# Optimization experiments

Measured on AMD Instinct MI355X. Metric: run time of the kernel, lower is better.

Reference implementation:

```python
import jax, jax.numpy as jnp
import numpy as np
from math import sqrt

L, H, D, HD, F, V, P = 8, 16, 1024, 64, 4096, 32000, 2048
B, S = 2, 2048
EPS = 1e-5


def _ln(x, g, b):
    m = jnp.mean(x, axis=-1, keepdims=True)
    v = jnp.mean((x - m) ** 2, axis=-1, keepdims=True)
    return (x - m) * jax.lax.rsqrt(v + EPS) * g + b


def setup_inputs() -> dict:
    key = jax.random.key(0)
    ks = jax.random.split(key, 12)
    w = 0.02
    return {
        'input_ids': jax.random.randint(ks[0], (B, S), 0, V),
        'tok_emb': jax.random.normal(ks[1], (V, D), jnp.float32) * w,
        'pos_emb': jax.random.normal(ks[2], (P, D), jnp.float32) * w,
        'emb_g': jnp.ones((D,), jnp.float32),
        'emb_b': jnp.zeros((D,), jnp.float32),
        'ln1_g': jnp.ones((L, D), jnp.float32),
        'ln1_b': jnp.zeros((L, D), jnp.float32),
        'ln2_g': jnp.ones((L, D), jnp.float32),
        'ln2_b': jnp.zeros((L, D), jnp.float32),
        'Wq': jax.random.normal(ks[3], (L, H, D, HD), jnp.float32) * w,
        'bq': jnp.zeros((L, H, HD), jnp.float32),
        'Wk': jax.random.normal(ks[4], (L, H, D, HD), jnp.float32) * w,
        'bk': jnp.zeros((L, H, HD), jnp.float32),
        'Wv': jax.random.normal(ks[5], (L, H, D, HD), jnp.float32) * w,
        'bv': jnp.zeros((L, H, HD), jnp.float32),
        'Wo': jax.random.normal(ks[6], (L, D, D), jnp.float32) * w,
        'bo': jnp.zeros((L, D), jnp.float32),
        'W1': jax.random.normal(ks[7], (L, D, F), jnp.float32) * w,
        'b1': jnp.zeros((L, F), jnp.float32),
        'W2': jax.random.normal(ks[8], (L, F, D), jnp.float32) * w,
        'b2': jnp.zeros((L, D), jnp.float32),
    }


def _encoder(input_ids, tok_emb, pos_emb, emb_g, emb_b, ln1_g, ln1_b, ln2_g,
             ln2_b, Wq, bq, Wk, bk, Wv, bv, Wo, bo, W1, b1, W2, b2):
    seq = input_ids.shape[-1]
    x = tok_emb[input_ids] + pos_emb[:seq][None, :, :]  # [B,S,D]
    x = _ln(x, emb_g, emb_b)  # dropout = identity (eval)

    scale = 1.0 / sqrt(HD)

    def layer(x, p):
        (g1, b1_, g2, b2_, wq, bq_, wk, bk_, wv, bv_, wo, bo_, w1, bb1, w2, bb2) = p
        h = _ln(x, g1, b1_)
        q = jnp.einsum('bsd,hdk->bhsk', h, wq) + bq_[:, None, :]
        k = jnp.einsum('bsd,hdk->bhsk', h, wk) + bk_[:, None, :]
        v = jnp.einsum('bsd,hdk->bhsk', h, wv) + bv_[:, None, :]
        scores = jnp.einsum('bhsk,bhtk->bhst', q, k) * scale
        w = jax.nn.softmax(scores, axis=-1)
        av = jnp.einsum('bhst,bhtk->bhsk', w, v)  # [B,H,S,hd]
        av = jnp.transpose(av, (0, 2, 1, 3)).reshape(x.shape[0], x.shape[1], D)
        x = x + jnp.einsum('bsd,de->bse', av, wo) + bo_
        h2 = _ln(x, g2, b2_)
        f = jax.nn.gelu(jnp.einsum('bsd,df->bsf', h2, w1) + bb1, approximate=False)
        x = x + jnp.einsum('bsf,fd->bsd', f, w2) + bb2
        return x, None

    xs = (ln1_g, ln1_b, ln2_g, ln2_b, Wq, bq, Wk, bk, Wv, bv, Wo, bo, W1, b1, W2, b2)
    x, _ = jax.lax.scan(layer, x, xs)
    return x


def reference(input_ids, tok_emb, pos_emb, emb_g, emb_b, ln1_g, ln1_b, ln2_g,
              ln2_b, Wq, bq, Wk, bk, Wv, bv, Wo, bo, W1, b1, W2, b2):
    return _encoder(input_ids, tok_emb, pos_emb, emb_g, emb_b, ln1_g, ln1_b,
                    ln2_g, ln2_b, Wq, bq, Wk, bk, Wv, bv, Wo, bo, W1, b1, W2, b2)
```

## Files before the change

### kernel.cpp

```cpp
#include <hip/hip_runtime.h>
#include <hip/hip_bf16.h>

#define L_ 8
#define H_ 16
#define D_ 1024
#define HD_ 64
#define F_ 4096
#define B_ 2
#define S_ 2048
#define NTOK (B_*S_)

typedef unsigned short u16;
typedef __bf16 bf16x8 __attribute__((ext_vector_type(8)));
typedef float f32x4 __attribute__((ext_vector_type(4)));

__device__ __forceinline__ u16 f2b(float f){ union{float f; unsigned u;} c; c.f = f; unsigned u = c.u; return (u16)((u + 0x7fffu + ((u>>16)&1u)) >> 16); }
__device__ __forceinline__ u16 f2b_fast(float f){ union{float f; unsigned u;} c; c.f = f; return (u16)((c.u + 0x8000u) >> 16); }
__device__ __forceinline__ float b2f(u16 x){ union{unsigned u; float f;} c; c.u = ((unsigned)x)<<16; return c.f; }

__device__ __forceinline__ void gload16(const u16* g, u16* l){
  __builtin_amdgcn_global_load_lds(
      (const __attribute__((address_space(1))) void*)g,
      (__attribute__((address_space(3))) void*)l,
      16 , 0 , 0 );
}

__device__ __forceinline__ void blk_reduce2(float& a, float& b, float* sm){
  for (int off=32; off>0; off>>=1){ a += __shfl_down(a,off); b += __shfl_down(b,off); }
  int w = threadIdx.x>>6, ln = threadIdx.x&63;
  if (ln==0){ sm[w]=a; sm[4+w]=b; }
  __syncthreads();
  a = sm[0]+sm[1]+sm[2]+sm[3];
  b = sm[4]+sm[5]+sm[6]+sm[7];
}

__global__ __launch_bounds__(256) void embed_ln(const int* __restrict__ ids,
    const float* __restrict__ tok, const float* __restrict__ pos,
    const float* __restrict__ g, const float* __restrict__ bb,
    float* __restrict__ x)
{
  __shared__ float sm[8];
  int row = blockIdx.x;
  int s   = row % S_;
  int id  = ids[row];
  const float* te = tok + (size_t)id * D_;
  const float* pe = pos + (size_t)s  * D_;
  float v[4]; float sum=0.f, sq=0.f;
  #pragma unroll
  for (int i=0;i<4;i++){ int d = threadIdx.x + i*256; v[i] = te[d] + pe[d]; sum += v[i]; sq += v[i]*v[i]; }
  blk_reduce2(sum, sq, sm);
  float mean = sum * (1.0f/D_);
  float var  = sq  * (1.0f/D_) - mean*mean;
  float inv  = rsqrtf(var + 1e-5f);
  #pragma unroll
  for (int i=0;i<4;i++){ int d = threadIdx.x + i*256; x[(size_t)row*D_ + d] = (v[i]-mean)*inv*g[d] + bb[d]; }
}

__global__ __launch_bounds__(256) void ln_f32_bf16(const float* __restrict__ x,
    const float* __restrict__ g, const float* __restrict__ bb, u16* __restrict__ out)
{
  __shared__ float sm[8];
  int row = blockIdx.x;
  const float* xr = x + (size_t)row*D_;
  float v[4]; float sum=0.f, sq=0.f;
  #pragma unroll
  for (int i=0;i<4;i++){ int d = threadIdx.x + i*256; v[i] = xr[d]; sum += v[i]; sq += v[i]*v[i]; }
  blk_reduce2(sum, sq, sm);
  float mean = sum * (1.0f/D_);
  float var  = sq  * (1.0f/D_) - mean*mean;
  float inv  = rsqrtf(var + 1e-5f);
  #pragma unroll
  for (int i=0;i<4;i++){ int d = threadIdx.x + i*256; out[(size_t)row*D_ + d] = f2b((v[i]-mean)*inv*g[d] + bb[d]); }
}

__global__ __launch_bounds__(256) void transpose_w(const float* __restrict__ src,
    u16* __restrict__ dst, int R, int C)
{
  __shared__ u16 tile[32][33];
  int c0 = blockIdx.x*32, r0 = blockIdx.y*32;
  int tx = threadIdx.x, ty = threadIdx.y;
  #pragma unroll
  for (int i=0;i<4;i++){
    int r = ty + i*8;
    tile[r][tx] = f2b(src[(size_t)(r0+r)*C + c0 + tx]);
  }
  __syncthreads();
  #pragma unroll
  for (int i=0;i<4;i++){
    int c = ty + i*8;
    dst[(size_t)(c0+c)*R + r0 + tx] = tile[tx][c];
  }
}

__global__ __launch_bounds__(256) void qkv_repack(const float* __restrict__ Wq,
    const float* __restrict__ Wk, const float* __restrict__ Wv,
    u16* __restrict__ dst, int layer)
{
  __shared__ u16 tile[32][33];
  int z = blockIdx.z; int which = z >> 4, h = z & 15;
  const float* W = (which==0) ? Wq : (which==1) ? Wk : Wv;
  const float* src = W + ((size_t)(layer*H_ + h))*D_*HD_;
  int d0 = blockIdx.x*32, c0 = blockIdx.y*32;
  int tx = threadIdx.x, ty = threadIdx.y;
  #pragma unroll
  for (int i=0;i<4;i++){
    int r = ty + i*8;
    tile[r][tx] = f2b(src[(size_t)(d0+r)*HD_ + c0 + tx]);
  }
  __syncthreads();
  #pragma unroll
  for (int i=0;i<4;i++){
    int hd = c0 + ty + i*8;
    dst[(size_t)(which*1024 + h*64 + hd)*D_ + d0 + tx] = tile[tx][ty + i*8];
  }
}

__global__ __launch_bounds__(256) void v_transpose(const u16* __restrict__ qkv, u16* __restrict__ vT)
{
  __shared__ u16 tile[64*64];
  const int tt = blockIdx.x;
  const int bh = blockIdx.y;
  const int b = bh>>4, h = bh&15;
  const int t = threadIdx.x;
  const u16* src = qkv + (size_t)(b*S_ + tt*64)*3072 + 2048 + h*64;
  #pragma unroll
  for (int i=0;i<2;i++){
    int idx = t + i*256;
    int tl = idx>>3, hc = idx&7;
    uint4 v = *(const uint4*)(src + (size_t)tl*3072 + hc*8);
    *(uint4*)(&tile[tl*64 + ((hc ^ (tl&7))<<3)]) = v;
  }
  __syncthreads();
  u16* dst = vT + ((size_t)bh*64)*S_ + tt*64;
  #pragma unroll
  for (int i=0;i<2;i++){
    int idx = t + i*256;
    int hd = idx>>3, tc = idx&7;
    u16 tmp[8];
    #pragma unroll
    for (int j=0;j<8;j++){
      int tk = tc*8 + j;
      tmp[j] = tile[tk*64 + (hd ^ ((tk&7)<<3))];
    }
    *(uint4*)(dst + (size_t)hd*S_ + tc*8) = *(uint4*)tmp;
  }
}

__global__ __launch_bounds__(256) void gemm_bf16(
    const u16* __restrict__ A, const u16* __restrict__ Bt,
    const float* __restrict__ bias0, const float* __restrict__ bias1, const float* __restrict__ bias2,
    float* __restrict__ xres, u16* __restrict__ obf,
    int M, int N, int K, int epi)
{
  __shared__ u16 As[128*64];
  __shared__ u16 Bs[128*64];
  const int tid = threadIdx.x;
  const int nbx = gridDim.x;
  const int nwg = nbx * gridDim.y;
  int bid = blockIdx.x + nbx*blockIdx.y;
  int nid = (bid & 7)*(nwg >> 3) + (bid >> 3);
  const int bm = (nid % nbx) * 128;
  const int bn = (nid / nbx) * 128;
  const int wv = tid>>6, ln = tid&63;
  const int wr = wv>>1, wc = wv&1;
  const int l15 = ln&15, lhi = ln>>4;
  const int l8 = ln>>3;
  const int c8s = (ln&7) ^ l8;
  f32x4 acc[4][4];
  const f32x4 zero4 = {0.f,0.f,0.f,0.f};
  #pragma unroll
  for (int i=0;i<4;i++)
    #pragma unroll
    for (int j=0;j<4;j++) acc[i][j] = zero4;

  for (int k0 = 0; k0 < K; k0 += 64) {
    #pragma unroll
    for (int i=0;i<4;i++){
      int row = wv*8 + i*32 + l8;
      gload16(A  + (size_t)(bm+row)*K + k0 + c8s*8, &As[(wv*8 + i*32)*64]);
      gload16(Bt + (size_t)(bn+row)*K + k0 + c8s*8, &Bs[(wv*8 + i*32)*64]);
    }
    __syncthreads();
    #pragma unroll
    for (int ks=0; ks<2; ks++){
      bf16x8 af[4], bfr[4];
      #pragma unroll
      for (int i=0;i<4;i++){
        int ra = wr*64 + i*16 + l15;
        af[i]  = *(const bf16x8*)(&As[ra*64 + (((ks*4+lhi) ^ (ra&7))<<3)]);
        int rb = wc*64 + i*16 + l15;
        bfr[i] = *(const bf16x8*)(&Bs[rb*64 + (((ks*4+lhi) ^ (rb&7))<<3)]);
      }
      #pragma unroll
      for (int i=0;i<4;i++)
        #pragma unroll
        for (int j=0;j<4;j++)
          acc[i][j] = __builtin_amdgcn_mfma_f32_16x16x32_bf16(bfr[j], af[i], acc[i][j], 0,0,0);
    }
    __syncthreads();
  }

  #pragma unroll
  for (int j=0;j<4;j++){
    int col0 = bn + wc*64 + j*16 + lhi*4;
    float4 bv4;
    if (bias1){
      const float* bp = (col0 < 1024) ? (bias0 + col0)
                      : (col0 < 2048) ? (bias1 + col0 - 1024)
                                      : (bias2 + col0 - 2048);
      bv4 = *(const float4*)bp;
    } else {
      bv4 = *(const float4*)(bias0 + col0);
    }
    #pragma unroll
    for (int i=0;i<4;i++){
      int row = bm + wr*64 + i*16 + l15;
      size_t idx = (size_t)row*N + col0;
      float v0 = acc[i][j][0] + bv4.x;
      float v1 = acc[i][j][1] + bv4.y;
      float v2 = acc[i][j][2] + bv4.z;
      float v3 = acc[i][j][3] + bv4.w;
      if (epi==1){
        float4 t = *(float4*)(xres + idx);
        t.x += v0; t.y += v1; t.z += v2; t.w += v3;
        *(float4*)(xres + idx) = t;
      } else {
        if (epi==2){
          #define GELU_T(v) { float t2=(v)*(v); float u=(v)*fmaf(t2,0.044715f,1.0f); \
                              float e=exp2f(u*-2.3022082f); (v)=(v)*__builtin_amdgcn_rcpf(1.0f+e); }
          GELU_T(v0); GELU_T(v1); GELU_T(v2); GELU_T(v3);
          #undef GELU_T
        }
        uint2 w;
        w.x = (unsigned)f2b_fast(v0) | ((unsigned)f2b_fast(v1) << 16);
        w.y = (unsigned)f2b_fast(v2) | ((unsigned)f2b_fast(v3) << 16);
        *(uint2*)(obf + idx) = w;
      }
    }
  }
}

__global__ __launch_bounds__(256) void attn_fwd(const u16* __restrict__ qkv,
    const u16* __restrict__ vT, u16* __restrict__ att)
{
  __shared__ u16 Ks[2][64*64];
  __shared__ u16 Vs[2][64*64];
  const int tid = threadIdx.x, wv = tid>>6, ln = tid&63, l15 = ln&15, lhi = ln>>4;
  const int l8 = ln>>3;
  const int cs = (ln&7) ^ l8;
  int bid = blockIdx.x + 32*(blockIdx.y + 16*blockIdx.z);
  int nid = (bid & 7)*128 + (bid >> 3);
  const int qt = nid & 31, h = (nid >> 5) & 15, b = nid >> 9;
  const u16* qg = qkv + (size_t)b*S_*3072 + h*64;
  const u16* kg = qg + 1024;
  const u16* vtg = vT + ((size_t)(b*16 + h)*64)*S_;

  bf16x8 qf[2];
  {
    const u16* qrow = qg + (size_t)(qt*64 + wv*16 + l15)*3072;
    u16 tmp[16];
    *(uint4*)(tmp)   = *(const uint4*)(qrow + lhi*8);
    *(uint4*)(tmp+8) = *(const uint4*)(qrow + 32 + lhi*8);
    #pragma unroll
    for (int i=0;i<16;i++) tmp[i] = f2b_fast(b2f(tmp[i]) * 0.18033688f);
    qf[0] = *(const bf16x8*)(tmp);
    qf[1] = *(const bf16x8*)(tmp+8);
  }
  const f32x4 zero4 = {0.f,0.f,0.f,0.f};
  f32x4 oacc[4];
  #pragma unroll
  for (int j=0;j<4;j++) oacc[j] = zero4;
  float lsum = 0.f;

  #define STAGE_KV(bufi, kti) do {                                            \
    _Pragma("unroll")                                                         \
    for (int i_=0;i_<2;i_++){                                                 \
      int r0_ = wv*8 + i_*32;                                                 \
      int row_ = r0_ + l8;                                                    \
      gload16(kg  + (size_t)((kti)*64+row_)*3072 + cs*8, &Ks[bufi][r0_*64]);  \
      gload16(vtg + (size_t)row_*S_ + (kti)*64 + cs*8,   &Vs[bufi][r0_*64]);  \
    }                                                                         \
  } while(0)

  STAGE_KV(0, 0);
  __syncthreads();
  int buf = 0;

  for (int kt=0; kt<S_/64; kt++){
    if (kt+1 < S_/64) STAGE_KV(buf^1, kt+1);

    f32x4 s[4];
    __builtin_amdgcn_s_setprio(1);
    #pragma unroll
    for (int j=0;j<4;j++){
      s[j] = zero4;
      #pragma unroll
      for (int ks=0; ks<2; ks++){
        int kr = j*16 + l15;
        bf16x8 kf = *(const bf16x8*)(&Ks[buf][kr*64 + (((ks*4+lhi) ^ (kr&7))<<3)]);
        s[j] = __builtin_amdgcn_mfma_f32_16x16x32_bf16(kf, qf[ks], s[j], 0,0,0);
      }
    }
    __builtin_amdgcn_s_setprio(0);

    unsigned pk[8];
    float part = 0.f;
    #pragma unroll
    for (int j=0;j<4;j++){
      float p0 = exp2f(s[j][0]);
      float p1 = exp2f(s[j][1]);
      float p2 = exp2f(s[j][2]);
      float p3 = exp2f(s[j][3]);
      part += (p0+p1)+(p2+p3);
      asm("v_cvt_pk_bf16_f32 %0, %1, %2" : "=v"(pk[j*2])   : "v"(p0), "v"(p1));
      asm("v_cvt_pk_bf16_f32 %0, %1, %2" : "=v"(pk[j*2+1]) : "v"(p2), "v"(p3));
    }
    lsum += part;

    unsigned pw[2][4];
    #pragma unroll
    for (int ks=0; ks<2; ks++){
      #pragma unroll
      for (int w=0; w<4; w++){
        int src = l15 + (lhi&1)*32 + (w>>1)*16;
        unsigned a  = __shfl(pk[ks*4 + (w&1)],     src);
        unsigned bb = __shfl(pk[ks*4 + 2 + (w&1)], src);
        pw[ks][w] = (lhi & 2) ? bb : a;
      }
    }
    bf16x8 pf[2];
    #pragma unroll
    for (int ks=0; ks<2; ks++){
      union { unsigned u[4]; bf16x8 v; } pu;
      pu.u[0]=pw[ks][0]; pu.u[1]=pw[ks][1]; pu.u[2]=pw[ks][2]; pu.u[3]=pw[ks][3];
      pf[ks] = pu.v;
    }

    __builtin_amdgcn_s_setprio(1);
    #pragma unroll
    for (int dj=0; dj<4; dj++){
      #pragma unroll
      for (int ks=0; ks<2; ks++){
        int vr = dj*16 + l15;
        bf16x8 vf = *(const bf16x8*)(&Vs[buf][vr*64 + (((ks*4+lhi) ^ (vr&7))<<3)]);
        oacc[dj] = __builtin_amdgcn_mfma_f32_16x16x32_bf16(pf[ks], vf, oacc[dj], 0,0,0);
      }
    }
    __builtin_amdgcn_s_setprio(0);
    __syncthreads();
    buf ^= 1;
  }
  #undef STAGE_KV

  float tot = lsum + __shfl_xor(lsum, 16);
  tot += __shfl_xor(tot, 32);
  float inv[4];
  #pragma unroll
  for (int r=0;r<4;r++) inv[r] = __builtin_amdgcn_rcpf(__shfl(tot, lhi*4+r));

  #pragma unroll
  for (int dj=0; dj<4; dj++){
    #pragma unroll
    for (int r=0;r<4;r++){
      int q = lhi*4 + r;
      int token = qt*64 + wv*16 + q;
      att[(size_t)(b*S_ + token)*D_ + h*HD_ + dj*16 + l15] = f2b_fast(oacc[dj][r] * inv[r]);
    }
  }
}

extern "C" void kernel_launch(void* const* d_in, const int* in_sizes, int n_in,
                              void* d_out, int out_size, void* d_ws, size_t ws_size,
                              hipStream_t stream)
{
  const int*   ids   = (const int*)d_in[0];
  const float* tok   = (const float*)d_in[1];
  const float* pos   = (const float*)d_in[2];
  const float* emb_g = (const float*)d_in[3];
  const float* emb_b = (const float*)d_in[4];
  const float* ln1g  = (const float*)d_in[5];
  const float* ln1b  = (const float*)d_in[6];
  const float* ln2g  = (const float*)d_in[7];
  const float* ln2b  = (const float*)d_in[8];
  const float* Wq = (const float*)d_in[9];
  const float* bq = (const float*)d_in[10];
  const float* Wk = (const float*)d_in[11];
  const float* bk = (const float*)d_in[12];
  const float* Wv = (const float*)d_in[13];
  const float* bv = (const float*)d_in[14];
  const float* Wo = (const float*)d_in[15];
  const float* bo = (const float*)d_in[16];
  const float* W1 = (const float*)d_in[17];
  const float* b1 = (const float*)d_in[18];
  const float* W2 = (const float*)d_in[19];
  const float* b2 = (const float*)d_in[20];

  float* x = (float*)d_out;
  char* ws = (char*)d_ws;
  u16* h     = (u16*)(ws);
  u16* qkvb  = (u16*)(ws + 8388608);
  u16* att   = (u16*)(ws + 33554432);
  u16* fbuf  = (u16*)(ws + 41943040);
  u16* vT    = fbuf;
  u16* wqkvt = (u16*)(ws + 75497472);
  u16* wot   = (u16*)(ws + 81788928);
  u16* w1t   = (u16*)(ws + 83886080);
  u16* w2t   = (u16*)(ws + 92274688);

  embed_ln<<<NTOK, 256, 0, stream>>>(ids, tok, pos, emb_g, emb_b, x);

  for (int l=0; l<L_; l++){
    ln_f32_bf16<<<NTOK, 256, 0, stream>>>(x, ln1g + l*D_, ln1b + l*D_, h);
    qkv_repack<<<dim3(32,2,48), dim3(32,8), 0, stream>>>(Wq, Wk, Wv, wqkvt, l);
    gemm_bf16<<<dim3(32,24), 256, 0, stream>>>(h, wqkvt,
        bq + l*1024, bk + l*1024, bv + l*1024,
        nullptr, qkvb, NTOK, 3072, 1024, 0);
    v_transpose<<<dim3(32,32), 256, 0, stream>>>(qkvb, vT);
    attn_fwd<<<dim3(S_/64, H_, B_), 256, 0, stream>>>(qkvb, vT, att);
    transpose_w<<<dim3(32,32), dim3(32,8), 0, stream>>>(Wo + (size_t)l*D_*D_, wot, D_, D_);
    gemm_bf16<<<dim3(32,8), 256, 0, stream>>>(att, wot,
        bo + l*D_, nullptr, nullptr,
        x, nullptr, NTOK, 1024, 1024, 1);
    ln_f32_bf16<<<NTOK, 256, 0, stream>>>(x, ln2g + l*D_, ln2b + l*D_, h);
    transpose_w<<<dim3(128,32), dim3(32,8), 0, stream>>>(W1 + (size_t)l*D_*F_, w1t, D_, F_);
    gemm_bf16<<<dim3(32,32), 256, 0, stream>>>(h, w1t,
        b1 + l*F_, nullptr, nullptr,
        nullptr, fbuf, NTOK, 4096, 1024, 2);
    transpose_w<<<dim3(32,128), dim3(32,8), 0, stream>>>(W2 + (size_t)l*F_*D_, w2t, F_, D_);
    gemm_bf16<<<dim3(32,8), 256, 0, stream>>>(fbuf, w2t,
        b2 + l*D_, nullptr, nullptr,
        x, nullptr, NTOK, 1024, 4096, 1);
  }
}
```

Baseline: 2.541 ms.

## Add double-buffered 256x256 GEMM kernel for QKV and FFN1 projections

Introduces a 512-thread GEMM with 256x256 output tiles and two LDS buffers. It prefetches the next K-slice with direct global-to-LDS loads while MFMA runs on the current one, with fine-grained vmcnt waits and barriers between quadrant phases. It replaces the 128x128 kernel for the QKV and W1 projections to raise operand reuse per LDS load and overlap memory with compute. The trade-offs are a large LDS footprint and far fewer workgroups: 192 for QKV, which may underfill the CUs.

```diff
diff --git a/kernel.cpp b/kernel.cpp
--- a/kernel.cpp
+++ b/kernel.cpp
@@ -25,6 +25,12 @@
       16 , 0 , 0 );
 }
 
+#define WAITV_BAR(n) do { \
+  asm volatile("s_waitcnt vmcnt(%0)" :: "i"(n) : "memory"); \
+  __builtin_amdgcn_sched_barrier(0); \
+  __builtin_amdgcn_s_barrier(); \
+} while(0)
+
 __device__ __forceinline__ void blk_reduce2(float& a, float& b, float* sm){
   for (int off=32; off>0; off>>=1){ a += __shfl_down(a,off); b += __shfl_down(b,off); }
   int w = threadIdx.x>>6, ln = threadIdx.x&63;
@@ -143,6 +149,27 @@
       tmp[j] = tile[tk*64 + (hd ^ ((tk&7)<<3))];
     }
     *(uint4*)(dst + (size_t)hd*S_ + tc*8) = *(uint4*)tmp;
+  }
+}
+
+__device__ __forceinline__ void epi_store(float v0,float v1,float v2,float v3,
+    float* xres, u16* obf, size_t idx, int epi)
+{
+  if (epi==1){
+    float4 t = *(float4*)(xres + idx);
+    t.x += v0; t.y += v1; t.z += v2; t.w += v3;
+    *(float4*)(xres + idx) = t;
+  } else {
+    if (epi==2){
+      #define GELU_T(v) { float t2=(v)*(v); float u=(v)*fmaf(t2,0.044715f,1.0f); \
+                          float e=exp2f(u*-2.3022082f); (v)=(v)*__builtin_amdgcn_rcpf(1.0f+e); }
+      GELU_T(v0); GELU_T(v1); GELU_T(v2); GELU_T(v3);
+      #undef GELU_T
+    }
+    uint2 w;
+    w.x = (unsigned)f2b_fast(v0) | ((unsigned)f2b_fast(v1) << 16);
+    w.y = (unsigned)f2b_fast(v2) | ((unsigned)f2b_fast(v3) << 16);
+    *(uint2*)(obf + idx) = w;
   }
 }
 
@@ -215,29 +242,134 @@
     #pragma unroll
     for (int i=0;i<4;i++){
       int row = bm + wr*64 + i*16 + l15;
-      size_t idx = (size_t)row*N + col0;
-      float v0 = acc[i][j][0] + bv4.x;
-      float v1 = acc[i][j][1] + bv4.y;
-      float v2 = acc[i][j][2] + bv4.z;
-      float v3 = acc[i][j][3] + bv4.w;
-      if (epi==1){
-        float4 t = *(float4*)(xres + idx);
-        t.x += v0; t.y += v1; t.z += v2; t.w += v3;
-        *(float4*)(xres + idx) = t;
+      epi_store(acc[i][j][0]+bv4.x, acc[i][j][1]+bv4.y, acc[i][j][2]+bv4.z, acc[i][j][3]+bv4.w,
+                xres, obf, (size_t)row*N + col0, epi);
+    }
+  }
+}
+
+__global__ __launch_bounds__(512) void gemm256(
+    const u16* __restrict__ A, const u16* __restrict__ Bt,
+    const float* __restrict__ bias0, const float* __restrict__ bias1, const float* __restrict__ bias2,
+    float* __restrict__ xres, u16* __restrict__ obf,
+    int M, int N, int K, int epi)
+{
+  __shared__ u16 As[2][256*64];
+  __shared__ u16 Bs[2][256*64];
+  const int tid = threadIdx.x;
+  const int nbx = gridDim.x;
+  const int nwg = nbx * gridDim.y;
+  int bid = blockIdx.x + nbx*blockIdx.y;
+  int nid = (bid & 7)*(nwg >> 3) + (bid >> 3);
+  const int bm = (nid % nbx) * 256;
+  const int bn = (nid / nbx) * 256;
+  const int wv = tid>>6, ln = tid&63;
+  const int wm = wv>>2, wn = wv&3;
+  const int l15 = ln&15, lhi = ln>>4;
+  const int l8 = ln>>3;
+  const int c8s = (ln&7) ^ l8;
+
+  f32x4 acc[2][2][4][2];
+  const f32x4 zero4 = {0.f,0.f,0.f,0.f};
+  #pragma unroll
+  for (int a=0;a<2;a++) for (int b=0;b<2;b++)
+    #pragma unroll
+    for (int i=0;i<4;i++) for (int j=0;j<2;j++) acc[a][b][i][j] = zero4;
+
+  const u16* aB0 = A  + (size_t)(bm + wv*16 + l8)*K + c8s*8;
+  const u16* bB0 = Bt + (size_t)(bn + wv*16 + l8)*K + c8s*8;
+
+  #define ISSUE(c, kt) do {                                                  \
+    const u16* aB = aB0 + (size_t)(kt)*64;                                   \
+    const u16* bB = bB0 + (size_t)(kt)*64;                                   \
+    gload16(aB,               &As[c][(wv*16      )*64]);                     \
+    gload16(aB + (size_t)8*K, &As[c][(wv*16 +   8)*64]);                     \
+    gload16(bB,               &Bs[c][(wv*16      )*64]);                     \
+    gload16(bB + (size_t)8*K, &Bs[c][(wv*16 +   8)*64]);                     \
+    gload16(aB + (size_t)128*K, &As[c][(128 + wv*16    )*64]);               \
+    gload16(aB + (size_t)136*K, &As[c][(128 + wv*16 + 8)*64]);               \
+    gload16(bB + (size_t)128*K, &Bs[c][(128 + wv*16    )*64]);               \
+    gload16(bB + (size_t)136*K, &Bs[c][(128 + wv*16 + 8)*64]);               \
+  } while(0)
+
+  #define PHASE(c, qr, qc) do {                                              \
+    bf16x8 af[4][2], bfr[2][2];                                              \
+    _Pragma("unroll")                                                        \
+    for (int i=0;i<4;i++){                                                   \
+      int ra = (qr)*128 + wm*64 + i*16 + l15;                                \
+      _Pragma("unroll")                                                      \
+      for (int ks=0; ks<2; ks++)                                             \
+        af[i][ks] = *(const bf16x8*)(&As[c][ra*64 + (((ks*4+lhi) ^ (ra&7))<<3)]); \
+    }                                                                        \
+    _Pragma("unroll")                                                        \
+    for (int j=0;j<2;j++){                                                   \
+      int rb = (qc)*128 + wn*32 + j*16 + l15;                                \
+      _Pragma("unroll")                                                      \
+      for (int ks=0; ks<2; ks++)                                             \
+        bfr[j][ks] = *(const bf16x8*)(&Bs[c][rb*64 + (((ks*4+lhi) ^ (rb&7))<<3)]); \
+    }                                                                        \
+    __builtin_amdgcn_s_setprio(1);                                           \
+    _Pragma("unroll")                                                        \
+    for (int ks=0; ks<2; ks++)                                               \
+      _Pragma("unroll")                                                      \
+      for (int i=0;i<4;i++)                                                  \
+        _Pragma("unroll")                                                    \
+        for (int j=0;j<2;j++)                                                \
+          acc[qr][qc][i][j] = __builtin_amdgcn_mfma_f32_16x16x32_bf16(       \
+              bfr[j][ks], af[i][ks], acc[qr][qc][i][j], 0,0,0);              \
+    __builtin_amdgcn_s_setprio(0);                                           \
+  } while(0)
+
+  const int nt = K >> 6;
+  ISSUE(0, 0);
+  WAITV_BAR(4);
+  for (int t=0; t<nt-1; ++t){
+    int c = t&1;
+    ISSUE(c^1, t+1);
+    PHASE(c, 0, 0);
+    WAITV_BAR(10);
+    PHASE(c, 1, 0);
+    WAITV_BAR(8);
+    PHASE(c, 0, 1);
+    PHASE(c, 1, 1);
+    WAITV_BAR(4);
+  }
+  {
+    int c = (nt-1)&1;
+    PHASE(c, 0, 0);
+    WAITV_BAR(2);
+    PHASE(c, 1, 0);
+    WAITV_BAR(0);
+    PHASE(c, 0, 1);
+    PHASE(c, 1, 1);
+  }
+  #undef ISSUE
+  #undef PHASE
+
+  #pragma unroll
+  for (int qc=0; qc<2; qc++)
+    #pragma unroll
+    for (int j=0;j<2;j++){
+      int col0 = bn + qc*128 + wn*32 + j*16 + lhi*4;
+      float4 bv4;
+      if (bias1){
+        const float* bp = (col0 < 1024) ? (bias0 + col0)
+                        : (col0 < 2048) ? (bias1 + col0 - 1024)
+                                        : (bias2 + col0 - 2048);
+        bv4 = *(const float4*)bp;
       } else {
-        if (epi==2){
-          #define GELU_T(v) { float t2=(v)*(v); float u=(v)*fmaf(t2,0.044715f,1.0f); \
-                              float e=exp2f(u*-2.3022082f); (v)=(v)*__builtin_amdgcn_rcpf(1.0f+e); }
-          GELU_T(v0); GELU_T(v1); GELU_T(v2); GELU_T(v3);
-          #undef GELU_T
+        bv4 = *(const float4*)(bias0 + col0);
+      }
+      #pragma unroll
+      for (int qr=0; qr<2; qr++)
+        #pragma unroll
+        for (int i=0;i<4;i++){
+          int row = bm + qr*128 + wm*64 + i*16 + l15;
+          epi_store(acc[qr][qc][i][j][0]+bv4.x, acc[qr][qc][i][j][1]+bv4.y,
+                    acc[qr][qc][i][j][2]+bv4.z, acc[qr][qc][i][j][3]+bv4.w,
+                    xres, obf, (size_t)row*N + col0, epi);
         }
-        uint2 w;
-        w.x = (unsigned)f2b_fast(v0) | ((unsigned)f2b_fast(v1) << 16);
-        w.y = (unsigned)f2b_fast(v2) | ((unsigned)f2b_fast(v3) << 16);
-        *(uint2*)(obf + idx) = w;
-      }
-    }
-  }
+    }
 }
 
 __global__ __launch_bounds__(256) void attn_fwd(const u16* __restrict__ qkv,
@@ -412,7 +544,7 @@
   for (int l=0; l<L_; l++){
     ln_f32_bf16<<<NTOK, 256, 0, stream>>>(x, ln1g + l*D_, ln1b + l*D_, h);
     qkv_repack<<<dim3(32,2,48), dim3(32,8), 0, stream>>>(Wq, Wk, Wv, wqkvt, l);
-    gemm_bf16<<<dim3(32,24), 256, 0, stream>>>(h, wqkvt,
+    gemm256<<<dim3(16,12), 512, 0, stream>>>(h, wqkvt,
         bq + l*1024, bk + l*1024, bv + l*1024,
         nullptr, qkvb, NTOK, 3072, 1024, 0);
     v_transpose<<<dim3(32,32), 256, 0, stream>>>(qkvb, vT);
@@ -423,7 +555,7 @@
         x, nullptr, NTOK, 1024, 1024, 1);
     ln_f32_bf16<<<NTOK, 256, 0, stream>>>(x, ln2g + l*D_, ln2b + l*D_, h);
     transpose_w<<<dim3(128,32), dim3(32,8), 0, stream>>>(W1 + (size_t)l*D_*F_, w1t, D_, F_);
-    gemm_bf16<<<dim3(32,32), 256, 0, stream>>>(h, w1t,
+    gemm256<<<dim3(16,16), 512, 0, stream>>>(h, w1t,
         b1 + l*F_, nullptr, nullptr,
         nullptr, fbuf, NTOK, 4096, 1024, 2);
     transpose_w<<<dim3(32,128), dim3(32,8), 0, stream>>>(W2 + (size_t)l*F_*D_, w2t, F_, D_);
```

Measured after the change: 2.504 ms. About the same (-1.4%).
